# Kernel optimization log

Measured on AMD Instinct MI355X. Metric: run time of the kernel, lower is better.

The kernel has to match this reference:

```python
import jax, jax.numpy as jnp
import numpy as np
import math

NEG = -10000.0  # original uses -10000.0, not -inf

def setup_inputs() -> dict:
    key = jax.random.key(0)
    B, S, H, D = 2, 2048, 16, 128
    qkv = jax.random.normal(key, (B, S, 3, H, D), dtype=jnp.float32)
    return {"qkv": qkv}

def reference(qkv):
    # qkv: (B, S, 3, H, D); causal softmax attention, dropout p=0 (identity)
    B, S, _, H, D = qkv.shape
    q = qkv[:, :, 0]  # (B,S,H,D)
    k = qkv[:, :, 1]
    v = qkv[:, :, 2]
    softmax_scale = 1.0 / math.sqrt(D)
    # scores: (B, H, T, S)
    scores = jnp.einsum('bthd,bshd->bhts', q, k * softmax_scale)
    causal_mask = jnp.triu(jnp.full((S, S), NEG, dtype=scores.dtype), 1)
    scores = scores + causal_mask  # broadcast over (B,H)
    attention = jax.nn.softmax(scores, axis=-1)
    out = jnp.einsum('bhts,bshd->bthd', attention, v)  # (B,T,H,D)
    return out
```

## Files before the change

### kernel.cpp

```cpp
#include <hip/hip_runtime.h>
#include <hip/hip_bf16.h>
#include <math.h>

typedef __bf16 bf16;
typedef bf16 bf16x8 __attribute__((ext_vector_type(8)));
typedef float floatx4 __attribute__((ext_vector_type(4)));

#define MFMA16(a, b, c) __builtin_amdgcn_mfma_f32_16x16x32_bf16(a, b, c, 0, 0, 0)

constexpr int Bb = 2, Ss = 2048, Hh = 16, Dd = 128;
constexpr float SCALE = 0.08838834764831845f;

__global__ __launch_bounds__(256) void prep_pack(const float* __restrict__ qkv,
                                                 bf16* __restrict__ QP,
                                                 bf16* __restrict__ KP,
                                                 bf16* __restrict__ VP) {
  __shared__ bf16 Vt[64 * 136];

  const int tid = threadIdx.x;
  const int w = tid >> 6, lane = tid & 63, quad = lane >> 4, l15 = lane & 15;
  const int qt = blockIdx.x, bh = blockIdx.y;
  const int b = bh >> 4, h = bh & 15;
  const int q0 = qt * 64;
  const size_t rs = (size_t)3 * Hh * Dd;
  const float* base = qkv + (size_t)b * Ss * rs + (size_t)h * Dd;

  for (int idx = tid; idx < 64 * 32; idx += 256) {
    const int row = idx >> 5;
    const int c4 = (idx & 31) << 2;
    const float* p = base + (size_t)(q0 + row) * rs + 2 * Hh * Dd + c4;
    float4 x = *(const float4*)p;
    bf16* d = Vt + row * 136 + c4;
    d[0] = (bf16)x.x; d[1] = (bf16)x.y; d[2] = (bf16)x.z; d[3] = (bf16)x.w;
  }

  {
    bf16* blob = QP + (size_t)(bh * 32 + qt) * 8192;
    const float* src = base + (size_t)(q0 + 4 * l15 + w) * rs;
    for (int kk = 0; kk < 4; ++kk) {
      const float* s8 = src + kk * 32 + quad * 8;
      float4 x0 = *(const float4*)s8, x1 = *(const float4*)(s8 + 4);
      bf16x8 f;
      f[0] = (bf16)(x0.x * SCALE); f[1] = (bf16)(x0.y * SCALE);
      f[2] = (bf16)(x0.z * SCALE); f[3] = (bf16)(x0.w * SCALE);
      f[4] = (bf16)(x1.x * SCALE); f[5] = (bf16)(x1.y * SCALE);
      f[6] = (bf16)(x1.z * SCALE); f[7] = (bf16)(x1.w * SCALE);
      *(bf16x8*)(blob + (size_t)(((w * 4 + kk) * 4 + quad) * 16 + l15) * 8) = f;
    }
  }

  const int ktg = qt * 2 + (w >> 1);
  {
    const int c = w & 1;
    bf16* blob = KP + (size_t)(bh * 64 + ktg) * 4096;
    const float* src = base + (size_t)(ktg * 32 + c * 16 + l15) * rs + Hh * Dd;
    for (int kk = 0; kk < 4; ++kk) {
      const float* s8 = src + kk * 32 + quad * 8;
      float4 x0 = *(const float4*)s8, x1 = *(const float4*)(s8 + 4);
      bf16x8 f;
      f[0] = (bf16)x0.x; f[1] = (bf16)x0.y; f[2] = (bf16)x0.z; f[3] = (bf16)x0.w;
      f[4] = (bf16)x1.x; f[5] = (bf16)x1.y; f[6] = (bf16)x1.z; f[7] = (bf16)x1.w;
      *(bf16x8*)(blob + (size_t)(((c * 4 + kk) * 4 + quad) * 16 + l15) * 8) = f;
    }
  }

  __syncthreads();

  {
    bf16* blob = VP + (size_t)(bh * 64 + ktg) * 4096;
    const int kloc = (w >> 1) * 32;
    for (int ti = 0; ti < 4; ++ti) {
      const int t = (w & 1) * 4 + ti;
      const int d = t * 16 + l15;
      bf16x8 f;
      for (int j = 0; j < 8; ++j) f[j] = Vt[(kloc + quad * 8 + j) * 136 + d];
      *(bf16x8*)(blob + (size_t)((t * 4 + quad) * 16 + l15) * 8) = f;
    }
  }
}

__device__ __forceinline__ void cp1k(const bf16* src, bf16* dst, int lane) {
  __builtin_amdgcn_global_load_lds(
      (__attribute__((address_space(1))) void*)(src + lane * 8),
      (__attribute__((address_space(3))) void*)dst, 16, 0, 0);
}

__global__ __launch_bounds__(256, 3) void attn_fwd(const bf16* __restrict__ QP,
                                                   const bf16* __restrict__ KP,
                                                   const bf16* __restrict__ VP,
                                                   float* __restrict__ out) {
  __shared__ bf16 Kl[2][4096];
  __shared__ bf16 Vl[2][4096];
  __shared__ bf16 Pl[4 * 32 * 40];

  const int tid = threadIdx.x;
  const int w = tid >> 6, lane = tid & 63, quad = lane >> 4, l15 = lane & 15;
  const int qt = (gridDim.x - 1) - blockIdx.x;
  const int bh = blockIdx.y;
  const int b = bh >> 4, h = bh & 15;
  const int q0 = qt * 128;

  bf16x8 qf[2][4];
  for (int u = 0; u < 2; ++u) {
    const bf16* qp = QP + (size_t)(bh * 32 + 2 * qt + u) * 8192;
    for (int kk = 0; kk < 4; ++kk)
      qf[u][kk] = *(const bf16x8*)(qp + (size_t)(((w * 4 + kk) * 4 + quad) * 16 + l15) * 8);
  }

  floatx4 acc_o[2][8];
  for (int u = 0; u < 2; ++u)
    for (int t = 0; t < 8; ++t) acc_o[u][t] = (floatx4){0.f, 0.f, 0.f, 0.f};
  float l_part[2][4] = {{0.f, 0.f, 0.f, 0.f}, {0.f, 0.f, 0.f, 0.f}};

  const int ntiles = 4 * qt + 4;
  const size_t bh64 = (size_t)bh * 64;
  bf16* pw = &Pl[w * 1280];

  auto stage = [&](int kt, int nb) {
    const bf16* kblob = KP + (bh64 + kt) * 4096;
    const bf16* vblob = VP + (bh64 + kt) * 4096;
    if (w < 2) {
      for (int i = 0; i < 4; ++i) {
        const int g = w * 4 + i;
        cp1k(kblob + g * 512, &Kl[nb][g * 512], lane);
      }
    } else {
      for (int i = 0; i < 4; ++i) {
        const int g = (w - 2) * 4 + i;
        cp1k(vblob + g * 512, &Vl[nb][g * 512], lane);
      }
    }
  };

  stage(0, 0);
  __syncthreads();

  for (int kt = 0; kt < ntiles; ++kt) {
    const int nb = kt & 1;
    if (kt + 1 < ntiles) stage(kt + 1, nb ^ 1);

    const bool do0 = (kt <= 4 * qt + 1);
    const bool mask0 = (kt >= 4 * qt);
    const bool mask1 = (kt >= 4 * qt + 2);
    const int kbase = kt * 32;

    floatx4 s0[2], s1[2];
    s0[0] = s0[1] = s1[0] = s1[1] = (floatx4){0.f, 0.f, 0.f, 0.f};
    for (int c = 0; c < 2; ++c)
      for (int kk = 0; kk < 4; ++kk) {
        bf16x8 bfrag = *(const bf16x8*)(&Kl[nb][((c * 4 + kk) * 64 + lane) * 8]);
        if (do0) s0[c] = MFMA16(qf[0][kk], bfrag, s0[c]);
        s1[c] = MFMA16(qf[1][kk], bfrag, s1[c]);
      }

    if (do0) {
      float p[2][4];
      if (mask0) {
        for (int c = 0; c < 2; ++c) {
          const int colg = kbase + c * 16 + l15;
          for (int r = 0; r < 4; ++r) {
            const int rowg = q0 + 4 * (quad * 4 + r) + w;
            p[c][r] = __expf((colg > rowg) ? -10000.f : s0[c][r]);
          }
        }
      } else {
        for (int c = 0; c < 2; ++c)
          for (int r = 0; r < 4; ++r) p[c][r] = __expf(s0[c][r]);
      }
      for (int r = 0; r < 4; ++r) l_part[0][r] += p[0][r] + p[1][r];
      for (int c = 0; c < 2; ++c)
        for (int r = 0; r < 4; ++r)
          pw[(quad * 4 + r) * 40 + c * 16 + l15] = (bf16)p[c][r];
    }
    {
      float p[2][4];
      if (mask1) {
        for (int c = 0; c < 2; ++c) {
          const int colg = kbase + c * 16 + l15;
          for (int r = 0; r < 4; ++r) {
            const int rowg = q0 + 64 + 4 * (quad * 4 + r) + w;
            p[c][r] = __expf((colg > rowg) ? -10000.f : s1[c][r]);
          }
        }
      } else {
        for (int c = 0; c < 2; ++c)
          for (int r = 0; r < 4; ++r) p[c][r] = __expf(s1[c][r]);
      }
      for (int r = 0; r < 4; ++r) l_part[1][r] += p[0][r] + p[1][r];
      for (int c = 0; c < 2; ++c)
        for (int r = 0; r < 4; ++r)
          pw[(16 + quad * 4 + r) * 40 + c * 16 + l15] = (bf16)p[c][r];
    }

    bf16x8 af0, af1;
    if (do0) af0 = *(const bf16x8*)(&Pl[w * 1280 + l15 * 40 + quad * 8]);
    af1 = *(const bf16x8*)(&Pl[w * 1280 + (16 + l15) * 40 + quad * 8]);
    for (int t = 0; t < 8; ++t) {
      bf16x8 vfrag = *(const bf16x8*)(&Vl[nb][(t * 64 + lane) * 8]);
      if (do0) acc_o[0][t] = MFMA16(af0, vfrag, acc_o[0][t]);
      acc_o[1][t] = MFMA16(af1, vfrag, acc_o[1][t]);
    }

    __syncthreads();
  }

  for (int u = 0; u < 2; ++u) {
    float rl[4];
    for (int r = 0; r < 4; ++r) {
      float l = l_part[u][r];
      for (int off = 1; off < 16; off <<= 1) l += __shfl_xor(l, off);
      rl[r] = 1.0f / l;
    }
    for (int r = 0; r < 4; ++r) {
      const int rowg = q0 + u * 64 + 4 * (quad * 4 + r) + w;
      float* op = out + ((size_t)(b * Ss + rowg) * Hh + h) * Dd + l15;
      for (int t = 0; t < 8; ++t) op[t * 16] = acc_o[u][t][r] * rl[r];
    }
  }
}

extern "C" void kernel_launch(void* const* d_in, const int* in_sizes, int n_in,
                              void* d_out, int out_size, void* d_ws, size_t ws_size,
                              hipStream_t stream) {
  const float* qkv = (const float*)d_in[0];
  float* out = (float*)d_out;
  bf16* QP = (bf16*)d_ws;
  bf16* KP = QP + (size_t)8 * 1024 * 1024;
  bf16* VP = KP + (size_t)8 * 1024 * 1024;

  prep_pack<<<dim3(32, 32), 256, 0, stream>>>(qkv, QP, KP, VP);
  attn_fwd<<<dim3(16, 32), 256, 0, stream>>>(QP, KP, VP, out);
}
```

Before: 250.5 us.

## Split long causal query tiles across KV chunks with a merge kernel

Long query tiles get split into 2-4 KV-range chunks via constant lookup tables, so the grid grows from 16 to 40 blocks per head with more balanced work per block. Partial unnormalized outputs (bf16) and row sums go to workspace, and a new reduce_merge kernel sums the chunks and normalizes. This is meant to remove the load imbalance and tail left by the triangular causal workload. The cost is an extra launch, extra global traffic for the partials, and bf16 rounding of partial outputs. A fallback to the original monolithic kernel is kept for when the workspace is too small.

```diff
diff --git a/kernel.cpp b/kernel.cpp
--- a/kernel.cpp
+++ b/kernel.cpp
@@ -10,6 +10,16 @@
 
 constexpr int Bb = 2, Ss = 2048, Hh = 16, Dd = 128;
 constexpr float SCALE = 0.08838834764831845f;
+
+__constant__ int U_QT[40] = {0,1,2,3, 4,4, 5,5, 6,6, 7,7, 8,8,8, 9,9,9, 10,10,10,
+                             11,11,11, 12,12,12,12, 13,13,13,13, 14,14,14,14, 15,15,15,15};
+__constant__ int U_S[40]  = {0,0,0,0, 0,10, 0,12, 0,14, 0,16, 0,12,24, 0,14,27, 0,15,30,
+                             0,16,32, 0,13,26,39, 0,14,28,42, 0,15,30,45, 0,16,32,48};
+__constant__ int U_E[40]  = {4,8,12,16, 10,20, 12,24, 14,28, 16,32, 12,24,36, 14,27,40,
+                             15,30,44, 16,32,48, 13,26,39,52, 14,28,42,56, 15,30,45,60,
+                             16,32,48,64};
+__constant__ int RS0[12] = {0,2,4,6,8,11,14,17,20,24,28,32};
+__constant__ int RN[12]  = {2,2,2,2,3,3,3,3,4,4,4,4};
 
 __global__ __launch_bounds__(256) void prep_pack(const float* __restrict__ qkv,
                                                  bf16* __restrict__ QP,
@@ -85,34 +95,37 @@
       (__attribute__((address_space(3))) void*)dst, 16, 0, 0);
 }
 
-__global__ __launch_bounds__(256, 3) void attn_fwd(const bf16* __restrict__ QP,
-                                                   const bf16* __restrict__ KP,
-                                                   const bf16* __restrict__ VP,
-                                                   float* __restrict__ out) {
+__global__ __launch_bounds__(256, 3) void attn_fwd_s(const bf16* __restrict__ QP,
+                                                     const bf16* __restrict__ KP,
+                                                     const bf16* __restrict__ VP,
+                                                     float* __restrict__ out,
+                                                     bf16* __restrict__ PO,
+                                                     float* __restrict__ PL) {
   __shared__ bf16 Kl[2][4096];
   __shared__ bf16 Vl[2][4096];
   __shared__ bf16 Pl[4 * 32 * 40];
 
   const int tid = threadIdx.x;
   const int w = tid >> 6, lane = tid & 63, quad = lane >> 4, l15 = lane & 15;
-  const int qt = (gridDim.x - 1) - blockIdx.x;
+  const int u = blockIdx.x;
   const int bh = blockIdx.y;
   const int b = bh >> 4, h = bh & 15;
+  const int qt = U_QT[u];
+  const int ks = U_S[u], ke = U_E[u];
   const int q0 = qt * 128;
 
   bf16x8 qf[2][4];
-  for (int u = 0; u < 2; ++u) {
-    const bf16* qp = QP + (size_t)(bh * 32 + 2 * qt + u) * 8192;
+  for (int m = 0; m < 2; ++m) {
+    const bf16* qp = QP + (size_t)(bh * 32 + 2 * qt + m) * 8192;
     for (int kk = 0; kk < 4; ++kk)
-      qf[u][kk] = *(const bf16x8*)(qp + (size_t)(((w * 4 + kk) * 4 + quad) * 16 + l15) * 8);
+      qf[m][kk] = *(const bf16x8*)(qp + (size_t)(((w * 4 + kk) * 4 + quad) * 16 + l15) * 8);
   }
 
   floatx4 acc_o[2][8];
-  for (int u = 0; u < 2; ++u)
-    for (int t = 0; t < 8; ++t) acc_o[u][t] = (floatx4){0.f, 0.f, 0.f, 0.f};
+  for (int m = 0; m < 2; ++m)
+    for (int t = 0; t < 8; ++t) acc_o[m][t] = (floatx4){0.f, 0.f, 0.f, 0.f};
   float l_part[2][4] = {{0.f, 0.f, 0.f, 0.f}, {0.f, 0.f, 0.f, 0.f}};
 
-  const int ntiles = 4 * qt + 4;
   const size_t bh64 = (size_t)bh * 64;
   bf16* pw = &Pl[w * 1280];
 
@@ -132,12 +145,12 @@
     }
   };
 
-  stage(0, 0);
+  stage(ks, 0);
   __syncthreads();
 
-  for (int kt = 0; kt < ntiles; ++kt) {
-    const int nb = kt & 1;
-    if (kt + 1 < ntiles) stage(kt + 1, nb ^ 1);
+  for (int it = 0, kt = ks; kt < ke; ++kt, ++it) {
+    const int nb = it & 1;
+    if (kt + 1 < ke) stage(kt + 1, nb ^ 1);
 
     const bool do0 = (kt <= 4 * qt + 1);
     const bool mask0 = (kt >= 4 * qt);
@@ -204,17 +217,205 @@
     __syncthreads();
   }
 
-  for (int u = 0; u < 2; ++u) {
+  if (u < 4) {
+    for (int m = 0; m < 2; ++m) {
+      float rl[4];
+      for (int r = 0; r < 4; ++r) {
+        float l = l_part[m][r];
+        for (int off = 1; off < 16; off <<= 1) l += __shfl_xor(l, off);
+        rl[r] = 1.0f / l;
+      }
+      for (int r = 0; r < 4; ++r) {
+        const int rowg = q0 + m * 64 + 4 * (quad * 4 + r) + w;
+        float* op = out + ((size_t)(b * Ss + rowg) * Hh + h) * Dd + l15;
+        for (int t = 0; t < 8; ++t) op[t * 16] = acc_o[m][t][r] * rl[r];
+      }
+    }
+  } else {
+    const int slot = bh * 36 + (u - 4);
+    bf16* po = PO + (size_t)slot * 16384;
+    float* pl = PL + (size_t)slot * 128;
+    for (int m = 0; m < 2; ++m) {
+      for (int r = 0; r < 4; ++r) {
+        float l = l_part[m][r];
+        for (int off = 1; off < 16; off <<= 1) l += __shfl_xor(l, off);
+        if (l15 == 0) pl[m * 64 + 4 * (quad * 4 + r) + w] = l;
+      }
+      for (int r = 0; r < 4; ++r) {
+        const int rloc = m * 64 + 4 * (quad * 4 + r) + w;
+        bf16* pp = po + rloc * 128 + l15;
+        for (int t = 0; t < 8; ++t) pp[t * 16] = (bf16)acc_o[m][t][r];
+      }
+    }
+  }
+}
+
+__global__ __launch_bounds__(256) void reduce_merge(const bf16* __restrict__ PO,
+                                                    const float* __restrict__ PL,
+                                                    float* __restrict__ out) {
+  const int qt = 4 + blockIdx.x;
+  const int bh = blockIdx.y;
+  const int b = bh >> 4, h = bh & 15;
+  const int s0 = bh * 36 + RS0[blockIdx.x];
+  const int nch = RN[blockIdx.x];
+  const int tid = threadIdx.x;
+
+  __shared__ float linv[128];
+  if (tid < 128) {
+    float l = 0.f;
+    for (int c = 0; c < nch; ++c) l += PL[(size_t)(s0 + c) * 128 + tid];
+    linv[tid] = 1.0f / l;
+  }
+  __syncthreads();
+
+  const int q0 = qt * 128;
+  for (int t = 0; t < 32; ++t) {
+    const int idx2 = t * 256 + tid;
+    const int row = idx2 >> 6;
+    const int d = (idx2 & 63) * 2;
+    float v0 = 0.f, v1 = 0.f;
+    for (int c = 0; c < nch; ++c) {
+      const bf16* p = PO + (size_t)(s0 + c) * 16384 + row * 128 + d;
+      v0 += (float)p[0];
+      v1 += (float)p[1];
+    }
+    float* op = out + ((size_t)(b * Ss + q0 + row) * Hh + h) * Dd + d;
+    const float rl = linv[row];
+    op[0] = v0 * rl;
+    op[1] = v1 * rl;
+  }
+}
+
+__global__ __launch_bounds__(256, 3) void attn_fwd_mono(const bf16* __restrict__ QP,
+                                                        const bf16* __restrict__ KP,
+                                                        const bf16* __restrict__ VP,
+                                                        float* __restrict__ out) {
+  __shared__ bf16 Kl[2][4096];
+  __shared__ bf16 Vl[2][4096];
+  __shared__ bf16 Pl[4 * 32 * 40];
+
+  const int tid = threadIdx.x;
+  const int w = tid >> 6, lane = tid & 63, quad = lane >> 4, l15 = lane & 15;
+  const int qt = (gridDim.x - 1) - blockIdx.x;
+  const int bh = blockIdx.y;
+  const int b = bh >> 4, h = bh & 15;
+  const int q0 = qt * 128;
+
+  bf16x8 qf[2][4];
+  for (int m = 0; m < 2; ++m) {
+    const bf16* qp = QP + (size_t)(bh * 32 + 2 * qt + m) * 8192;
+    for (int kk = 0; kk < 4; ++kk)
+      qf[m][kk] = *(const bf16x8*)(qp + (size_t)(((w * 4 + kk) * 4 + quad) * 16 + l15) * 8);
+  }
+
+  floatx4 acc_o[2][8];
+  for (int m = 0; m < 2; ++m)
+    for (int t = 0; t < 8; ++t) acc_o[m][t] = (floatx4){0.f, 0.f, 0.f, 0.f};
+  float l_part[2][4] = {{0.f, 0.f, 0.f, 0.f}, {0.f, 0.f, 0.f, 0.f}};
+
+  const int ntiles = 4 * qt + 4;
+  const size_t bh64 = (size_t)bh * 64;
+  bf16* pw = &Pl[w * 1280];
+
+  auto stage = [&](int kt, int nb) {
+    const bf16* kblob = KP + (bh64 + kt) * 4096;
+    const bf16* vblob = VP + (bh64 + kt) * 4096;
+    if (w < 2) {
+      for (int i = 0; i < 4; ++i) {
+        const int g = w * 4 + i;
+        cp1k(kblob + g * 512, &Kl[nb][g * 512], lane);
+      }
+    } else {
+      for (int i = 0; i < 4; ++i) {
+        const int g = (w - 2) * 4 + i;
+        cp1k(vblob + g * 512, &Vl[nb][g * 512], lane);
+      }
+    }
+  };
+
+  stage(0, 0);
+  __syncthreads();
+
+  for (int kt = 0; kt < ntiles; ++kt) {
+    const int nb = kt & 1;
+    if (kt + 1 < ntiles) stage(kt + 1, nb ^ 1);
+
+    const bool do0 = (kt <= 4 * qt + 1);
+    const bool mask0 = (kt >= 4 * qt);
+    const bool mask1 = (kt >= 4 * qt + 2);
+    const int kbase = kt * 32;
+
+    floatx4 s0[2], s1[2];
+    s0[0] = s0[1] = s1[0] = s1[1] = (floatx4){0.f, 0.f, 0.f, 0.f};
+    for (int c = 0; c < 2; ++c)
+      for (int kk = 0; kk < 4; ++kk) {
+        bf16x8 bfrag = *(const bf16x8*)(&Kl[nb][((c * 4 + kk) * 64 + lane) * 8]);
+        if (do0) s0[c] = MFMA16(qf[0][kk], bfrag, s0[c]);
+        s1[c] = MFMA16(qf[1][kk], bfrag, s1[c]);
+      }
+
+    if (do0) {
+      float p[2][4];
+      if (mask0) {
+        for (int c = 0; c < 2; ++c) {
+          const int colg = kbase + c * 16 + l15;
+          for (int r = 0; r < 4; ++r) {
+            const int rowg = q0 + 4 * (quad * 4 + r) + w;
+            p[c][r] = __expf((colg > rowg) ? -10000.f : s0[c][r]);
+          }
+        }
+      } else {
+        for (int c = 0; c < 2; ++c)
+          for (int r = 0; r < 4; ++r) p[c][r] = __expf(s0[c][r]);
+      }
+      for (int r = 0; r < 4; ++r) l_part[0][r] += p[0][r] + p[1][r];
+      for (int c = 0; c < 2; ++c)
+        for (int r = 0; r < 4; ++r)
+          pw[(quad * 4 + r) * 40 + c * 16 + l15] = (bf16)p[c][r];
+    }
+    {
+      float p[2][4];
+      if (mask1) {
+        for (int c = 0; c < 2; ++c) {
+          const int colg = kbase + c * 16 + l15;
+          for (int r = 0; r < 4; ++r) {
+            const int rowg = q0 + 64 + 4 * (quad * 4 + r) + w;
+            p[c][r] = __expf((colg > rowg) ? -10000.f : s1[c][r]);
+          }
+        }
+      } else {
+        for (int c = 0; c < 2; ++c)
+          for (int r = 0; r < 4; ++r) p[c][r] = __expf(s1[c][r]);
+      }
+      for (int r = 0; r < 4; ++r) l_part[1][r] += p[0][r] + p[1][r];
+      for (int c = 0; c < 2; ++c)
+        for (int r = 0; r < 4; ++r)
+          pw[(16 + quad * 4 + r) * 40 + c * 16 + l15] = (bf16)p[c][r];
+    }
+
+    bf16x8 af0, af1;
+    if (do0) af0 = *(const bf16x8*)(&Pl[w * 1280 + l15 * 40 + quad * 8]);
+    af1 = *(const bf16x8*)(&Pl[w * 1280 + (16 + l15) * 40 + quad * 8]);
+    for (int t = 0; t < 8; ++t) {
+      bf16x8 vfrag = *(const bf16x8*)(&Vl[nb][(t * 64 + lane) * 8]);
+      if (do0) acc_o[0][t] = MFMA16(af0, vfrag, acc_o[0][t]);
+      acc_o[1][t] = MFMA16(af1, vfrag, acc_o[1][t]);
+    }
+
+    __syncthreads();
+  }
+
+  for (int m = 0; m < 2; ++m) {
     float rl[4];
     for (int r = 0; r < 4; ++r) {
-      float l = l_part[u][r];
+      float l = l_part[m][r];
       for (int off = 1; off < 16; off <<= 1) l += __shfl_xor(l, off);
       rl[r] = 1.0f / l;
     }
     for (int r = 0; r < 4; ++r) {
-      const int rowg = q0 + u * 64 + 4 * (quad * 4 + r) + w;
+      const int rowg = q0 + m * 64 + 4 * (quad * 4 + r) + w;
       float* op = out + ((size_t)(b * Ss + rowg) * Hh + h) * Dd + l15;
-      for (int t = 0; t < 8; ++t) op[t * 16] = acc_o[u][t][r] * rl[r];
+      for (int t = 0; t < 8; ++t) op[t * 16] = acc_o[m][t][r] * rl[r];
     }
   }
 }
@@ -224,10 +425,20 @@
                               hipStream_t stream) {
   const float* qkv = (const float*)d_in[0];
   float* out = (float*)d_out;
-  bf16* QP = (bf16*)d_ws;
-  bf16* KP = QP + (size_t)8 * 1024 * 1024;
-  bf16* VP = KP + (size_t)8 * 1024 * 1024;
+  char* ws = (char*)d_ws;
+  bf16* QP = (bf16*)ws;
+  bf16* KP = (bf16*)(ws + (size_t)16 * 1024 * 1024);
+  bf16* VP = (bf16*)(ws + (size_t)32 * 1024 * 1024);
+  bf16* PO = (bf16*)(ws + (size_t)48 * 1024 * 1024);
+  float* PL = (float*)(ws + (size_t)48 * 1024 * 1024 + (size_t)1152 * 32768);
+
+  const size_t need = (size_t)48 * 1024 * 1024 + (size_t)1152 * 32768 + (size_t)1152 * 512;
 
   prep_pack<<<dim3(32, 32), 256, 0, stream>>>(qkv, QP, KP, VP);
-  attn_fwd<<<dim3(16, 32), 256, 0, stream>>>(QP, KP, VP, out);
-}
+  if (ws_size >= need) {
+    attn_fwd_s<<<dim3(40, 32), 256, 0, stream>>>(QP, KP, VP, out, PO, PL);
+    reduce_merge<<<dim3(12, 32), 256, 0, stream>>>(PO, PL, out);
+  } else {
+    attn_fwd_mono<<<dim3(16, 32), 256, 0, stream>>>(QP, KP, VP, out);
+  }
+}
```

New measurement: 259.8 us. +3.7%, slower.
